# Optimization experiments

Measured on AMD Instinct MI355X. Metric: run time of the kernel, lower is better.

The kernel has to match this reference:

```python
import jax, jax.numpy as jnp
import numpy as np
import math

B, L, DIM = 128, 192, 512
NTOKEN = 100
MAX_BONDS = 6
MAX_LEN = 192


def _sinusoidal_pe(max_len, dim):
    pos = np.arange(max_len, dtype=np.float32)[:, None]
    div = np.exp(np.arange(0, dim, 2, dtype=np.float32) * (-math.log(10000.0) / dim))
    pe = np.zeros((max_len, dim), dtype=np.float32)
    pe[:, 0::2] = np.sin(pos * div)
    pe[:, 1::2] = np.cos(pos * div)
    return jnp.asarray(pe[:, None, :])  # [max_len, 1, dim]


def setup_inputs() -> dict:
    key = jax.random.key(0)
    ks = jax.random.split(key, 16)
    s = 0.02
    inp = {
        "element": jax.random.randint(ks[0], (B, L), 0, NTOKEN),
        "bond": jax.random.randint(ks[1], (B, L, MAX_BONDS), 0, L),
        "aroma": jax.random.randint(ks[2], (B, L), 0, 2),
        "charge": jax.random.randint(ks[3], (B, L), 0, 6),
        "segment": jax.random.randint(ks[4], (B, L), 0, 30),
        # parameters
        "pe": _sinusoidal_pe(MAX_LEN, DIM),
        "E_elem": jax.random.normal(ks[5], (NTOKEN, DIM), jnp.float32) * s,
        "E_charge": jax.random.normal(ks[6], (13, DIM), jnp.float32) * s,
        "E_aroma": jax.random.normal(ks[7], (2, DIM), jnp.float32) * s,
        "E_seg": jax.random.normal(ks[8], (30, DIM), jnp.float32) * s,
        "W1": jax.random.normal(ks[9], (DIM, 4 * DIM), jnp.float32) * s,
        "b1": jnp.zeros((4 * DIM,), jnp.float32),
        "W2": jax.random.normal(ks[10], (4 * DIM, DIM), jnp.float32) * s,
        "b2": jnp.zeros((DIM,), jnp.float32),
        "W3": jax.random.normal(ks[11], (DIM, 4 * DIM), jnp.float32) * s,
        "b3": jnp.zeros((4 * DIM,), jnp.float32),
        "W4": jax.random.normal(ks[12], (4 * DIM, DIM), jnp.float32) * s,
        "b4": jnp.zeros((DIM,), jnp.float32),
        "W5": jax.random.normal(ks[13], (DIM, DIM), jnp.float32) * s,
        "b5": jnp.zeros((DIM,), jnp.float32),
    }
    return inp


def _mlp(x, W1, b1, W2, b2, W3, b3, W4, b4, W5, b5):
    x = x + jnp.maximum(x @ W1 + b1, 0.0) @ W2 + b2
    x = x + jnp.maximum(x @ W3 + b3, 0.0) @ W4 + b4
    return x @ W5 + b5


def reference(element, bond, aroma, charge, segment, pe,
              E_elem, E_charge, E_aroma, E_seg,
              W1, b1, W2, b2, W3, b3, W4, b4, W5, b5):
    b, l = element.shape
    # embeddings: all [l, b, dim]
    emb = E_elem[element.T]
    emb = emb + pe[:l]                      # [l,1,dim] broadcast (eval: dropout off)
    emb = emb + E_aroma[aroma.T]
    emb = emb + E_charge[charge.T + 6]
    emb = emb + E_seg[segment.T]
    message = _mlp(emb, W1, b1, W2, b2, W3, b3, W4, b4, W5, b5)  # [l,b,dim]
    # bond aggregation: agg[k] = sum_m message[bond[b,k,m]] excluding self-bonds
    # (equivalent to the dense one-hot einsum with the diagonal masked out)
    msg_bld = jnp.transpose(message, (1, 0, 2))          # [b,l,dim]
    g = msg_bld[jnp.arange(b)[:, None, None], bond]      # [b,l,MAX_BONDS,dim]
    mask = (bond != jnp.arange(l)[None, :, None]).astype(message.dtype)
    agg = jnp.einsum('bkmd,bkm->bkd', g, mask)           # [b,l,dim]
    return emb + jnp.transpose(agg, (1, 0, 2))           # [l,b,dim]
```

## Files before the change

### kernel.cpp

```cpp
#include <hip/hip_runtime.h>
#include <cstdint>
#include <cstddef>

typedef unsigned short u16;
typedef unsigned int u32;

typedef unsigned short u16x8 __attribute__((ext_vector_type(8)));
typedef __bf16 bf16x8 __attribute__((ext_vector_type(8)));
typedef float f32x4 __attribute__((ext_vector_type(4)));
typedef float f32x8 __attribute__((ext_vector_type(8)));

#define NB   128
#define NL   192
#define NTOK (NB * NL)
#define DIM  512
#define HID  2048

static __device__ __forceinline__ float bf2f(u16 h) {
    union { u32 u; float f; } v; v.u = ((u32)h) << 16; return v.f;
}
static __device__ __forceinline__ u16 f2bf(float f) {
    union { float f; u32 u; } v; v.f = f;
    u32 u = v.u + 0x7FFF + ((v.u >> 16) & 1);
    return (u16)(u >> 16);
}

__global__ void transpose_f2b(const float* __restrict__ in, u16* __restrict__ out,
                              int K, int N) {
    __shared__ float tile[32][33];
    int tx = threadIdx.x & 31, ty = threadIdx.x >> 5;
    int n0 = blockIdx.x * 32, k0 = blockIdx.y * 32;
#pragma unroll
    for (int i = 0; i < 4; i++)
        tile[ty + i * 8][tx] = in[(size_t)(k0 + ty + i * 8) * N + n0 + tx];
    __syncthreads();
#pragma unroll
    for (int i = 0; i < 4; i++)
        out[(size_t)(n0 + ty + i * 8) * K + k0 + tx] = f2bf(tile[tx][ty + i * 8]);
}

static __device__ __forceinline__ void add8f(float* acc, const float* p) {
    f32x8 v = *(const f32x8*)p;
#pragma unroll
    for (int i = 0; i < 8; i++) acc[i] += v[i];
}

__global__ void embed_kernel(const int* __restrict__ element, const int* __restrict__ aroma,
                             const int* __restrict__ charge, const int* __restrict__ segment,
                             const float* __restrict__ pe, const float* __restrict__ E_elem,
                             const float* __restrict__ E_charge, const float* __restrict__ E_aroma,
                             const float* __restrict__ E_seg,
                             float* __restrict__ emb32, u16* __restrict__ emb16) {
    int t = blockIdx.x * 4 + (threadIdx.x >> 6);
    int lane = threadIdx.x & 63;
    int l = t >> 7, b = t & 127;
    int d = lane * 8;
    int idx = b * NL + l;
    int e = element[idx];
    int a = aroma[idx];
    int c = charge[idx] + 6;
    int s = segment[idx];
    float acc[8] = {0, 0, 0, 0, 0, 0, 0, 0};
    add8f(acc, E_elem  + (size_t)e * DIM + d);
    add8f(acc, pe      + (size_t)l * DIM + d);
    add8f(acc, E_aroma + (size_t)a * DIM + d);
    add8f(acc, E_charge+ (size_t)c * DIM + d);
    add8f(acc, E_seg   + (size_t)s * DIM + d);
    f32x8 o32; u16x8 o16;
#pragma unroll
    for (int i = 0; i < 8; i++) { o32[i] = acc[i]; o16[i] = f2bf(acc[i]); }
    *(f32x8*)(emb32 + (size_t)t * DIM + d) = o32;
    *(u16x8*)(emb16 + (size_t)t * DIM + d) = o16;
}

__global__ __launch_bounds__(256, 2) void gemm_bt(
    const u16* __restrict__ A, const u16* __restrict__ BT,
    const float* __restrict__ bias, const u16* __restrict__ resid16,
    const float* __restrict__ resid32,
    u16* __restrict__ C, int M, int N, int K, int do_relu) {
    __shared__ __align__(16) u16 As[3][128 * 32];
    __shared__ __align__(16) u16 Bs[3][256 * 32];

    const int tid  = threadIdx.x;
    const int wave = tid >> 6;
    const int lane = tid & 63;
    const int m0 = blockIdx.x * 128;
    const int n0 = blockIdx.y * 256;
    const int wm = (wave >> 1) * 64;
    const int wn = (wave & 1) * 128;
    const int lr = lane >> 2;
    const int lc = (lane & 3) * 8;
    const int fr = lane & 15;
    const int fq = lane >> 4;

    f32x4 acc[4][8] = {};

    const u16* Ag0 = A  + (size_t)(m0 + wave * 16 + lr) * K + lc;
    const u16* Ag1 = Ag0 + (size_t)64 * K;
    const u16* Bg0 = BT + (size_t)(n0 + wave * 16 + lr) * K + lc;
    const u16* Bg1 = Bg0 + (size_t)64 * K;
    const u16* Bg2 = Bg0 + (size_t)128 * K;
    const u16* Bg3 = Bg0 + (size_t)192 * K;
    const int sA0 = (wave * 16) * 32;
    const int sA1 = (64 + wave * 16) * 32;
    const int sB0 = (wave * 16) * 32;
    const int sB1 = (64 + wave * 16) * 32;
    const int sB2 = (128 + wave * 16) * 32;
    const int sB3 = (192 + wave * 16) * 32;

#define GLL(gp, lp) __builtin_amdgcn_global_load_lds(                            \
        (const __attribute__((address_space(1))) void*)(gp),                     \
        (__attribute__((address_space(3))) void*)(lp), 16, 0, 0)
#define STAGE(buf, k0) do {                                                      \
    GLL(Ag0 + (k0), &As[buf][sA0]);                                              \
    GLL(Ag1 + (k0), &As[buf][sA1]);                                              \
    GLL(Bg0 + (k0), &Bs[buf][sB0]);                                              \
    GLL(Bg1 + (k0), &Bs[buf][sB1]);                                              \
    GLL(Bg2 + (k0), &Bs[buf][sB2]);                                              \
    GLL(Bg3 + (k0), &Bs[buf][sB3]);                                              \
} while (0)

    const int kIters = K >> 5;
    STAGE(0, 0);
    STAGE(1, 32);
    STAGE(2, 64);

    int cur = 0;
    for (int k = 0; k < kIters; ++k) {
        asm volatile("s_waitcnt vmcnt(12)\n\ts_barrier" ::: "memory");

        bf16x8 af[4], bg[8];
#pragma unroll
        for (int i = 0; i < 4; i++)
            af[i] = *(const bf16x8*)(&As[cur][(wm + i * 16 + fr) * 32 + fq * 8]);
#pragma unroll
        for (int j = 0; j < 8; j++)
            bg[j] = *(const bf16x8*)(&Bs[cur][(wn + j * 16 + fr) * 32 + fq * 8]);
#pragma unroll
        for (int i = 0; i < 4; i++)
#pragma unroll
            for (int j = 0; j < 8; j++)
                acc[i][j] = __builtin_amdgcn_mfma_f32_16x16x32_bf16(
                    af[i], bg[j], acc[i][j], 0, 0, 0);

        asm volatile("s_barrier" ::: "memory");
        const int knext = (k + 3 < kIters) ? (k + 3) << 5 : 0;
        STAGE(cur, knext);
        cur = (cur == 2) ? 0 : cur + 1;
    }
#undef STAGE
#undef GLL

#pragma unroll
    for (int j = 0; j < 8; j++) {
        int n = n0 + wn + j * 16 + fr;
        float bv = bias[n];
#pragma unroll
        for (int i = 0; i < 4; i++) {
#pragma unroll
            for (int r = 0; r < 4; r++) {
                int m = m0 + wm + i * 16 + fq * 4 + r;
                float v = acc[i][j][r] + bv;
                if (do_relu) v = fmaxf(v, 0.0f);
                if (resid16) v += bf2f(resid16[(size_t)m * N + n]);
                if (resid32) v += resid32[(size_t)m * N + n];
                C[(size_t)m * N + n] = f2bf(v);
            }
        }
    }
}

__global__ void agg_kernel(const float* __restrict__ emb32, const u16* __restrict__ msg,
                           const int* __restrict__ bond, float* __restrict__ out) {
    int t = blockIdx.x * 4 + (threadIdx.x >> 6);
    int lane = threadIdx.x & 63;
    int l = t >> 7, b = t & 127;
    int d = lane * 8;
    float acc[8];
    {
        f32x8 v = *(const f32x8*)(emb32 + (size_t)t * DIM + d);
#pragma unroll
        for (int i = 0; i < 8; i++) acc[i] = v[i];
    }
    const int* bp = bond + ((size_t)b * NL + l) * 6;
#pragma unroll
    for (int m = 0; m < 6; m++) {
        int j = bp[m];
        if (j != l) {
            u16x8 g = *(const u16x8*)(msg + ((size_t)j * NB + b) * DIM + d);
#pragma unroll
            for (int i = 0; i < 8; i++) acc[i] += bf2f(g[i]);
        }
    }
    f32x8 o;
#pragma unroll
    for (int i = 0; i < 8; i++) o[i] = acc[i];
    *(f32x8*)(out + (size_t)t * DIM + d) = o;
}

extern "C" void kernel_launch(void* const* d_in, const int* in_sizes, int n_in,
                              void* d_out, int out_size, void* d_ws, size_t ws_size,
                              hipStream_t stream) {
    const int* element = (const int*)d_in[0];
    const int* bond    = (const int*)d_in[1];
    const int* aroma   = (const int*)d_in[2];
    const int* charge  = (const int*)d_in[3];
    const int* segment = (const int*)d_in[4];
    const float* pe      = (const float*)d_in[5];
    const float* E_elem  = (const float*)d_in[6];
    const float* E_charge= (const float*)d_in[7];
    const float* E_aroma = (const float*)d_in[8];
    const float* E_seg   = (const float*)d_in[9];
    const float* W1 = (const float*)d_in[10];
    const float* b1 = (const float*)d_in[11];
    const float* W2 = (const float*)d_in[12];
    const float* b2 = (const float*)d_in[13];
    const float* W3 = (const float*)d_in[14];
    const float* b3 = (const float*)d_in[15];
    const float* W4 = (const float*)d_in[16];
    const float* b4 = (const float*)d_in[17];
    const float* W5 = (const float*)d_in[18];
    const float* b5 = (const float*)d_in[19];

    float* emb32 = (float*)d_out;

    char* ws = (char*)d_ws;
    size_t woff = 0;
    auto take = [&](size_t bytes) -> u16* {
        u16* p = (u16*)(ws + woff);
        woff += (bytes + 255) & ~(size_t)255;
        return p;
    };
    u16* W1T = take((size_t)HID * DIM * 2);
    u16* W2T = take((size_t)DIM * HID * 2);
    u16* W3T = take((size_t)HID * DIM * 2);
    u16* W4T = take((size_t)DIM * HID * 2);
    u16* W5T = take((size_t)DIM * DIM * 2);
    u16* emb16 = take((size_t)NTOK * DIM * 2);
    u16* msg   = take((size_t)NTOK * DIM * 2);

    static const int ncs[] = {1, 2, 3, 4, 6, 8, 12, 16, 24, 32, 48, 64, 96, 192};
    int CM = 128;
    for (int nc : ncs) {
        int cm = NTOK / nc;
        size_t need = woff + ((size_t)cm * HID * 2 + 256)
                           + ((size_t)cm * DIM * 2 + 256) * 2;
        if (need <= ws_size) { CM = cm; break; }
    }
    u16* hC  = take((size_t)CM * HID * 2);
    u16* xaC = take((size_t)CM * DIM * 2);
    u16* xbC = take((size_t)CM * DIM * 2);

    transpose_f2b<<<dim3(HID / 32, DIM / 32), 256, 0, stream>>>(W1, W1T, DIM, HID);
    transpose_f2b<<<dim3(DIM / 32, HID / 32), 256, 0, stream>>>(W2, W2T, HID, DIM);
    transpose_f2b<<<dim3(HID / 32, DIM / 32), 256, 0, stream>>>(W3, W3T, DIM, HID);
    transpose_f2b<<<dim3(DIM / 32, HID / 32), 256, 0, stream>>>(W4, W4T, HID, DIM);
    transpose_f2b<<<dim3(DIM / 32, DIM / 32), 256, 0, stream>>>(W5, W5T, DIM, DIM);

    embed_kernel<<<NTOK / 4, 256, 0, stream>>>(element, aroma, charge, segment, pe,
                                               E_elem, E_charge, E_aroma, E_seg,
                                               emb32, emb16);

    for (int c0 = 0; c0 < NTOK; c0 += CM) {
        const u16* x16 = emb16 + (size_t)c0 * DIM;
        const float* x32 = emb32 + (size_t)c0 * DIM;
        u16* msgC = msg + (size_t)c0 * DIM;
        gemm_bt<<<dim3(CM / 128, HID / 256), 256, 0, stream>>>(x16, W1T, b1, nullptr, nullptr, hC,  CM, HID, DIM, 1);
        gemm_bt<<<dim3(CM / 128, DIM / 256), 256, 0, stream>>>(hC,  W2T, b2, nullptr, x32,     xaC, CM, DIM, HID, 0);
        gemm_bt<<<dim3(CM / 128, HID / 256), 256, 0, stream>>>(xaC, W3T, b3, nullptr, nullptr, hC,  CM, HID, DIM, 1);
        gemm_bt<<<dim3(CM / 128, DIM / 256), 256, 0, stream>>>(hC,  W4T, b4, xaC,    nullptr,  xbC, CM, DIM, HID, 0);
        gemm_bt<<<dim3(CM / 128, DIM / 256), 256, 0, stream>>>(xbC, W5T, b5, nullptr, nullptr, msgC, CM, DIM, DIM, 0);
    }

    agg_kernel<<<NTOK / 4, 256, 0, stream>>>(emb32, msg, bond, (float*)d_out);
}
```

Before: 560.1 us.

## Replace async global-to-LDS triple buffering with register-staged padded double buffering

Drops the global_load_lds triple-buffered pipeline in the GEMM and instead prefetches the next K-tile into registers, then writes it to a double-buffered LDS tile with a padded row stride of 40 elements. The padding is meant to remove LDS bank conflicts on the fragment reads, and the register prefetch lets the global loads overlap with the MFMA work. The launch-bounds occupancy hint is removed, and B fragments are now loaded per column inside the MFMA loop, which lowers register pressure. It also skips chunk sizes that are not multiples of 128 when choosing the workspace chunk. The trade-off is extra VGPR use for the prefetch registers and a barrier wait on LDS writes every iteration.

```diff
diff --git a/kernel.cpp b/kernel.cpp
--- a/kernel.cpp
+++ b/kernel.cpp
@@ -15,6 +15,7 @@
 #define NTOK (NB * NL)
 #define DIM  512
 #define HID  2048
+#define LDSS 40
 
 static __device__ __forceinline__ float bf2f(u16 h) {
     union { u32 u; float f; } v; v.u = ((u32)h) << 16; return v.f;
@@ -73,13 +74,13 @@
     *(u16x8*)(emb16 + (size_t)t * DIM + d) = o16;
 }
 
-__global__ __launch_bounds__(256, 2) void gemm_bt(
+__global__ __launch_bounds__(256) void gemm_bt(
     const u16* __restrict__ A, const u16* __restrict__ BT,
     const float* __restrict__ bias, const u16* __restrict__ resid16,
     const float* __restrict__ resid32,
     u16* __restrict__ C, int M, int N, int K, int do_relu) {
-    __shared__ __align__(16) u16 As[3][128 * 32];
-    __shared__ __align__(16) u16 Bs[3][256 * 32];
+    __shared__ __align__(16) u16 As[2][128 * LDSS];
+    __shared__ __align__(16) u16 Bs[2][256 * LDSS];
 
     const int tid  = threadIdx.x;
     const int wave = tid >> 6;
@@ -101,55 +102,54 @@
     const u16* Bg1 = Bg0 + (size_t)64 * K;
     const u16* Bg2 = Bg0 + (size_t)128 * K;
     const u16* Bg3 = Bg0 + (size_t)192 * K;
-    const int sA0 = (wave * 16) * 32;
-    const int sA1 = (64 + wave * 16) * 32;
-    const int sB0 = (wave * 16) * 32;
-    const int sB1 = (64 + wave * 16) * 32;
-    const int sB2 = (128 + wave * 16) * 32;
-    const int sB3 = (192 + wave * 16) * 32;
-
-#define GLL(gp, lp) __builtin_amdgcn_global_load_lds(                            \
-        (const __attribute__((address_space(1))) void*)(gp),                     \
-        (__attribute__((address_space(3))) void*)(lp), 16, 0, 0)
-#define STAGE(buf, k0) do {                                                      \
-    GLL(Ag0 + (k0), &As[buf][sA0]);                                              \
-    GLL(Ag1 + (k0), &As[buf][sA1]);                                              \
-    GLL(Bg0 + (k0), &Bs[buf][sB0]);                                              \
-    GLL(Bg1 + (k0), &Bs[buf][sB1]);                                              \
-    GLL(Bg2 + (k0), &Bs[buf][sB2]);                                              \
-    GLL(Bg3 + (k0), &Bs[buf][sB3]);                                              \
-} while (0)
+    u16* wA0 = &As[0][(wave * 16 + lr) * LDSS + lc];
+    u16* wA1 = &As[0][(64 + wave * 16 + lr) * LDSS + lc];
+    u16* wB0 = &Bs[0][(wave * 16 + lr) * LDSS + lc];
+    u16* wB1 = &Bs[0][(64 + wave * 16 + lr) * LDSS + lc];
+    u16* wB2 = &Bs[0][(128 + wave * 16 + lr) * LDSS + lc];
+    u16* wB3 = &Bs[0][(192 + wave * 16 + lr) * LDSS + lc];
+    const int bufOffA = 128 * LDSS;
+    const int bufOffB = 256 * LDSS;
 
     const int kIters = K >> 5;
-    STAGE(0, 0);
-    STAGE(1, 32);
-    STAGE(2, 64);
-
-    int cur = 0;
+    u16x8 pa0 = *(const u16x8*)(Ag0);
+    u16x8 pa1 = *(const u16x8*)(Ag1);
+    u16x8 pb0 = *(const u16x8*)(Bg0);
+    u16x8 pb1 = *(const u16x8*)(Bg1);
+    u16x8 pb2 = *(const u16x8*)(Bg2);
+    u16x8 pb3 = *(const u16x8*)(Bg3);
+
     for (int k = 0; k < kIters; ++k) {
-        asm volatile("s_waitcnt vmcnt(12)\n\ts_barrier" ::: "memory");
-
-        bf16x8 af[4], bg[8];
+        const int cur = k & 1;
+        const int oA = cur * bufOffA, oB = cur * bufOffB;
+        *(u16x8*)(wA0 + oA) = pa0;
+        *(u16x8*)(wA1 + oA) = pa1;
+        *(u16x8*)(wB0 + oB) = pb0;
+        *(u16x8*)(wB1 + oB) = pb1;
+        *(u16x8*)(wB2 + oB) = pb2;
+        *(u16x8*)(wB3 + oB) = pb3;
+        const int kn = (k + 1 < kIters) ? (k + 1) << 5 : 0;
+        pa0 = *(const u16x8*)(Ag0 + kn);
+        pa1 = *(const u16x8*)(Ag1 + kn);
+        pb0 = *(const u16x8*)(Bg0 + kn);
+        pb1 = *(const u16x8*)(Bg1 + kn);
+        pb2 = *(const u16x8*)(Bg2 + kn);
+        pb3 = *(const u16x8*)(Bg3 + kn);
+        asm volatile("s_waitcnt lgkmcnt(0)\n\ts_barrier" ::: "memory");
+
+        bf16x8 af[4];
 #pragma unroll
         for (int i = 0; i < 4; i++)
-            af[i] = *(const bf16x8*)(&As[cur][(wm + i * 16 + fr) * 32 + fq * 8]);
-#pragma unroll
-        for (int j = 0; j < 8; j++)
-            bg[j] = *(const bf16x8*)(&Bs[cur][(wn + j * 16 + fr) * 32 + fq * 8]);
-#pragma unroll
-        for (int i = 0; i < 4; i++)
-#pragma unroll
-            for (int j = 0; j < 8; j++)
+            af[i] = *(const bf16x8*)(&As[cur][(wm + i * 16 + fr) * LDSS + fq * 8]);
+#pragma unroll
+        for (int j = 0; j < 8; j++) {
+            bf16x8 bg = *(const bf16x8*)(&Bs[cur][(wn + j * 16 + fr) * LDSS + fq * 8]);
+#pragma unroll
+            for (int i = 0; i < 4; i++)
                 acc[i][j] = __builtin_amdgcn_mfma_f32_16x16x32_bf16(
-                    af[i], bg[j], acc[i][j], 0, 0, 0);
-
-        asm volatile("s_barrier" ::: "memory");
-        const int knext = (k + 3 < kIters) ? (k + 3) << 5 : 0;
-        STAGE(cur, knext);
-        cur = (cur == 2) ? 0 : cur + 1;
-    }
-#undef STAGE
-#undef GLL
+                    af[i], bg, acc[i][j], 0, 0, 0);
+        }
+    }
 
 #pragma unroll
     for (int j = 0; j < 8; j++) {
@@ -243,6 +243,7 @@
     int CM = 128;
     for (int nc : ncs) {
         int cm = NTOK / nc;
+        if (cm % 128) continue;
         size_t need = woff + ((size_t)cm * HID * 2 + 256)
                            + ((size_t)cm * DIM * 2 + 256) * 2;
         if (need <= ws_size) { CM = cm; break; }
```

Measured after the change: 781.3 us. +39.5%, slower.
